# Kernel tuning notes

Measured on AMD Instinct MI355X. Metric: run time of the kernel, lower is better.

The kernel has to match this reference:

```python
import jax, jax.numpy as jnp
import numpy as np

N_DEC = 24        # num_hidden_layers * 2
IN_DIM = 768
HID = 128
OUT_DIM = 768 * 64 * 2 + 768 + 64  # 99136
BATCH = 64
GAIN = 1e-07


def _xavier(key, shape, gain):
    fan_in, fan_out = shape[-2], shape[-1]
    limit = gain * np.sqrt(6.0 / (fan_in + fan_out))
    return jax.random.uniform(key, shape, jnp.float32, -limit, limit)


def setup_inputs() -> dict:
    key = jax.random.key(0)
    k0, k1, k2 = jax.random.split(key, 3)
    x = jax.random.normal(k0, (BATCH, IN_DIM), jnp.float32)
    # stacked per-decoder weights (original: nn.ModuleList of N_DEC 2-layer MLPs)
    w1 = _xavier(k1, (N_DEC, IN_DIM, HID), GAIN)
    b1 = jnp.zeros((N_DEC, HID), jnp.float32)
    w2 = _xavier(k2, (N_DEC, HID, OUT_DIM), GAIN)
    b2 = jnp.zeros((N_DEC, OUT_DIM), jnp.float32)
    return {"hidden_inputs": x, "w1": w1, "b1": b1, "w2": w2, "b2": b2}


def reference(hidden_inputs, w1, b1, w2, b2):
    # Batched equivalent of the Python loop over N_DEC SimpleGenerators.
    # h: [n, b, hid]
    h = jax.nn.relu(jnp.einsum('bi,nih->nbh', hidden_inputs, w1) + b1[:, None, :])
    # out: [n, b, out_dim]  (original returns list of n arrays of shape [b, out_dim])
    out = jnp.einsum('nbh,nho->nbo', h, w2) + b2[:, None, :]
    return out
```

## Files before the change

### kernel.cpp

```cpp
#include <hip/hip_runtime.h>
#include <hip/hip_bf16.h>

#define N_DEC  24
#define IN_DIM 768
#define HID    128
#define ODIM   99136
#define BATCH  64
#define OTILE  256
#define NXBLK  ((ODIM + OTILE - 1) / OTILE)

typedef __attribute__((ext_vector_type(8))) short bf16x8;
typedef __attribute__((ext_vector_type(4))) float f32x4;

static __device__ __forceinline__ short f2bf_bits(float f) {
    union { __hip_bfloat16 b; short s; } u;
    u.b = __float2bfloat16(f);
    return u.s;
}

static __device__ __forceinline__ void gload_lds16(const float* src, float* dst) {
    __builtin_amdgcn_global_load_lds(
        (const __attribute__((address_space(1))) void*)src,
        (__attribute__((address_space(3))) void*)dst, 16, 0, 0);
}

__global__ __launch_bounds__(128) void gen_h_kernel(
    const float* __restrict__ x, const float* __restrict__ w1,
    const float* __restrict__ b1, __hip_bfloat16* __restrict__ hswz)
{
    const int nb = blockIdx.x;
    const int n  = nb >> 6;
    const int b  = nb & 63;
    const int t  = threadIdx.x;

    __shared__ float xs[IN_DIM];
    #pragma unroll
    for (int i = 0; i < IN_DIM / 128; ++i)
        xs[t + i * 128] = x[b * IN_DIM + t + i * 128];
    __syncthreads();

    const float* w = w1 + (size_t)n * IN_DIM * HID + t;
    float a0 = 0.f, a1 = 0.f, a2 = 0.f, a3 = 0.f;
    #pragma unroll 4
    for (int i = 0; i < IN_DIM; i += 4) {
        a0 = fmaf(xs[i + 0], w[(size_t)(i + 0) * HID], a0);
        a1 = fmaf(xs[i + 1], w[(size_t)(i + 1) * HID], a1);
        a2 = fmaf(xs[i + 2], w[(size_t)(i + 2) * HID], a2);
        a3 = fmaf(xs[i + 3], w[(size_t)(i + 3) * HID], a3);
    }
    float acc = (a0 + a1) + (a2 + a3) + b1[n * HID + t];
    acc = fmaxf(acc, 0.f);

    const int mt = b >> 4, lr = b & 15;
    const int ks = t >> 5, lg = (t >> 3) & 3, ii = t & 7;
    const size_t idx = (size_t)n * 8192
                     + (size_t)(((ks * 4 + mt) * 64) + lg * 16 + lr) * 8 + ii;
    hswz[idx] = __float2bfloat16(acc);
}

__global__ __launch_bounds__(256, 2) void gen_out_mfma(
    const __hip_bfloat16* __restrict__ hswz, const float* __restrict__ w2,
    const float* __restrict__ b2, float* __restrict__ out)
{
    const int n    = blockIdx.y;
    const int tid  = threadIdx.x;
    const int wave = tid >> 6;
    const int lane = tid & 63;
    const int lr   = lane & 15;
    const int lg   = lane >> 4;
    const long oblk = (long)blockIdx.x * OTILE;

    __shared__ float lds[2][32][256];

    const float* w2n = w2 + (size_t)n * HID * ODIM;

    auto stage = [&](int buf, int ks) {
        #pragma unroll
        for (int p = 0; p < 8; ++p) {
            const int r   = wave * 8 + p;
            const int swz = ((r >> 3) & 3) << 3;
            long col = oblk + ((lane * 4) ^ swz);
            if (col > ODIM - 4) col = ODIM - 4;
            gload_lds16(w2n + (size_t)(ks * 32 + r) * ODIM + col, &lds[buf][r][0]);
        }
    };

    stage(0, 0);

    const bf16x8* ha = (const bf16x8*)hswz + (size_t)n * 1024 + lane;
    bf16x8 a[4][4];
    #pragma unroll
    for (int mt = 0; mt < 4; ++mt)
        #pragma unroll
        for (int ks = 0; ks < 4; ++ks)
            a[mt][ks] = ha[(ks * 4 + mt) * 64];

    f32x4 bias4;
    const long ocol = oblk + wave * 64 + lr * 4;
    {
        long c = ocol;
        if (c > ODIM - 4) c = ODIM - 4;
        bias4 = *(const f32x4*)(b2 + (size_t)n * ODIM + c);
    }

    f32x4 acc[4][4];
    #pragma unroll
    for (int tt = 0; tt < 4; ++tt)
        #pragma unroll
        for (int mt = 0; mt < 4; ++mt)
            acc[tt][mt] = f32x4{0.f, 0.f, 0.f, 0.f};

    #pragma unroll
    for (int ks = 0; ks < 4; ++ks) {
        __builtin_amdgcn_s_barrier();
        if (ks < 3) {
            stage((ks + 1) & 1, ks + 1);
            asm volatile("s_waitcnt vmcnt(8)" ::: "memory");
        } else {
            asm volatile("s_waitcnt vmcnt(0)" ::: "memory");
        }
        __builtin_amdgcn_s_barrier();

        const int buf = ks & 1;
        #pragma unroll
        for (int tt = 0; tt < 4; ++tt) {
            const int csw = (wave * 64 + tt * 16 + lr) ^ (lg << 3);
            const float* lp = &lds[buf][lg * 8][csw];
            float bv[8];
            #pragma unroll
            for (int i = 0; i < 8; ++i)
                bv[i] = lp[(size_t)i * 256];
            bf16x8 bf;
            #pragma unroll
            for (int i = 0; i < 8; ++i)
                bf[i] = f2bf_bits(bv[i]);
            #pragma unroll
            for (int mt = 0; mt < 4; ++mt)
                acc[tt][mt] = __builtin_amdgcn_mfma_f32_16x16x32_bf16(
                                  a[mt][ks], bf, acc[tt][mt], 0, 0, 0);
        }
    }

    float* tb = &lds[0][0][0] + wave * 1024;
    float* ob = out + ((size_t)n * BATCH) * ODIM;
    const int rr = lane >> 4;

    #pragma unroll
    for (int mt = 0; mt < 4; ++mt) {
        #pragma unroll
        for (int tt = 0; tt < 4; ++tt)
            #pragma unroll
            for (int r = 0; r < 4; ++r)
                tb[(lg * 4 + r) * 64 + tt * 16 + lr] = acc[tt][mt][r];
        #pragma unroll
        for (int j = 0; j < 4; ++j) {
            f32x4 v = *(const f32x4*)&tb[(j * 4 + rr) * 64 + lr * 4];
            v += bias4;
            if (ocol <= ODIM - 4)
                *(f32x4*)(ob + (size_t)(mt * 16 + j * 4 + rr) * ODIM + ocol) = v;
        }
    }
}

extern "C" void kernel_launch(void* const* d_in, const int* in_sizes, int n_in,
                              void* d_out, int out_size, void* d_ws, size_t ws_size,
                              hipStream_t stream)
{
    const float* x  = (const float*)d_in[0];
    const float* w1 = (const float*)d_in[1];
    const float* b1 = (const float*)d_in[2];
    const float* w2 = (const float*)d_in[3];
    const float* b2 = (const float*)d_in[4];
    float* out = (float*)d_out;
    __hip_bfloat16* hbf = (__hip_bfloat16*)d_ws;

    gen_h_kernel<<<dim3(N_DEC * BATCH), dim3(128), 0, stream>>>(x, w1, b1, hbf);

    gen_out_mfma<<<dim3(NXBLK, N_DEC), dim3(256), 0, stream>>>(hbf, w2, b2, out);
}
```

Measured before the change: 376.5 us.

## Give each wave a private LDS slice of W2 and drop block barriers

The shared W2 staging tile is reorganized so each wave loads and consumes only its own 64-column slice, which lets the two block-wide barriers per k-step be removed in favor of per-wave vmcnt waits and a scheduling barrier. The epilogue transpose buffer also gets an XOR swizzle to reduce LDS bank conflicts. This aims to cut inter-wave synchronization stalls, but each wave now issues narrower 64-column loads per row and relies on per-wave ordering for correctness.

```diff
diff --git a/kernel.cpp b/kernel.cpp
--- a/kernel.cpp
+++ b/kernel.cpp
@@ -69,19 +69,21 @@
     const int lr   = lane & 15;
     const int lg   = lane >> 4;
     const long oblk = (long)blockIdx.x * OTILE;
+    const long wcol = oblk + wave * 64;
 
-    __shared__ float lds[2][32][256];
+    __shared__ float lds[2][4][32][64];
 
     const float* w2n = w2 + (size_t)n * HID * ODIM;
 
     auto stage = [&](int buf, int ks) {
         #pragma unroll
         for (int p = 0; p < 8; ++p) {
-            const int r   = wave * 8 + p;
+            const int r   = 4 * p + lg;
             const int swz = ((r >> 3) & 3) << 3;
-            long col = oblk + ((lane * 4) ^ swz);
-            if (col > ODIM - 4) col = ODIM - 4;
-            gload_lds16(w2n + (size_t)(ks * 32 + r) * ODIM + col, &lds[buf][r][0]);
+            const long col = wcol + ((lr * 4) ^ swz);
+            long c = col > (long)ODIM - 4 ? (long)ODIM - 4 : col;
+            gload_lds16(w2n + (size_t)(ks * 32 + r) * ODIM + c,
+                        &lds[buf][wave][4 * p][0]);
         }
     };
 
@@ -96,10 +98,9 @@
             a[mt][ks] = ha[(ks * 4 + mt) * 64];
 
     f32x4 bias4;
-    const long ocol = oblk + wave * 64 + lr * 4;
+    const long ocol = wcol + lr * 4;
     {
-        long c = ocol;
-        if (c > ODIM - 4) c = ODIM - 4;
+        long c = ocol > (long)ODIM - 4 ? (long)ODIM - 4 : ocol;
         bias4 = *(const f32x4*)(b2 + (size_t)n * ODIM + c);
     }
 
@@ -112,24 +113,23 @@
 
     #pragma unroll
     for (int ks = 0; ks < 4; ++ks) {
-        __builtin_amdgcn_s_barrier();
         if (ks < 3) {
             stage((ks + 1) & 1, ks + 1);
             asm volatile("s_waitcnt vmcnt(8)" ::: "memory");
         } else {
             asm volatile("s_waitcnt vmcnt(0)" ::: "memory");
         }
-        __builtin_amdgcn_s_barrier();
+        __builtin_amdgcn_sched_barrier(0);
 
         const int buf = ks & 1;
         #pragma unroll
         for (int tt = 0; tt < 4; ++tt) {
-            const int csw = (wave * 64 + tt * 16 + lr) ^ (lg << 3);
-            const float* lp = &lds[buf][lg * 8][csw];
+            const int csw = (tt * 16 + lr) ^ (lg << 3);
+            const float* lp = &lds[buf][wave][lg * 8][csw];
             float bv[8];
             #pragma unroll
             for (int i = 0; i < 8; ++i)
-                bv[i] = lp[(size_t)i * 256];
+                bv[i] = lp[(size_t)i * 64];
             bf16x8 bf;
             #pragma unroll
             for (int i = 0; i < 8; ++i)
@@ -141,7 +141,7 @@
         }
     }
 
-    float* tb = &lds[0][0][0] + wave * 1024;
+    float* tb = &lds[0][wave][0][0];
     float* ob = out + ((size_t)n * BATCH) * ODIM;
     const int rr = lane >> 4;
 
@@ -151,12 +151,12 @@
         for (int tt = 0; tt < 4; ++tt)
             #pragma unroll
             for (int r = 0; r < 4; ++r)
-                tb[(lg * 4 + r) * 64 + tt * 16 + lr] = acc[tt][mt][r];
+                tb[(lg * 4 + r) * 64 + ((tt * 16 + lr) ^ (lg << 3))] = acc[tt][mt][r];
         #pragma unroll
         for (int j = 0; j < 4; ++j) {
-            f32x4 v = *(const f32x4*)&tb[(j * 4 + rr) * 64 + lr * 4];
+            f32x4 v = *(const f32x4*)&tb[(j * 4 + rr) * 64 + ((lr * 4) ^ ((j & 3) << 3))];
             v += bias4;
-            if (ocol <= ODIM - 4)
+            if (ocol <= (long)ODIM - 4)
                 *(f32x4*)(ob + (size_t)(mt * 16 + j * 4 + rr) * ODIM + ocol) = v;
         }
     }
```

Result: no change. 372.8 us (-1.0%).
